# Performance work log

Hardware: AMD Instinct MI355X
Metric: run time of the kernel (lower is better)

Reference implementation:

```python
import jax, jax.numpy as jnp
import numpy as np

B, S, E, H = 4, 2048, 1024, 16
D = E // H


def setup_inputs() -> dict:
    key = jax.random.key(0)
    ks = jax.random.split(key, 8)
    inv = 1.0 / np.sqrt(E)
    return {
        "query": jax.random.normal(ks[0], (B, S, E), dtype=jnp.float32),
        "key": jax.random.normal(ks[1], (B, S, E), dtype=jnp.float32),
        "value": jax.random.normal(ks[2], (B, S, E), dtype=jnp.float32),
        "key_padding_mask": jnp.zeros((B, S), dtype=bool),
        "Wq": jax.random.uniform(ks[3], (E, E), jnp.float32, -inv, inv),
        "Wk": jax.random.uniform(ks[4], (E, E), jnp.float32, -inv, inv),
        "Wv": jax.random.uniform(ks[5], (E, E), jnp.float32, -inv, inv),
        "Wo": jax.random.uniform(ks[6], (E, E), jnp.float32, -inv, inv),
        "gamma": jnp.ones((H,), dtype=jnp.float32),
    }


def reference(query, key, value, key_padding_mask, Wq, Wk, Wv, Wo, gamma):
    b, s, e = query.shape
    h = gamma.shape[0]
    d = e // h
    # torch Linear: x @ W.T ; split into heads -> [b, h, s, d]
    q = (query @ Wq.T).reshape(b, s, h, d).swapaxes(1, 2)
    k = (key @ Wk.T).reshape(b, key.shape[1], h, d).swapaxes(1, 2)
    v = (value @ Wv.T).reshape(b, value.shape[1], h, d).swapaxes(1, 2)
    scores = jnp.einsum("bhqd,bhkd->bhqk", q, k) / jnp.sqrt(jnp.asarray(d, q.dtype))
    scores = jnp.where(key_padding_mask[:, None, None, :], -jnp.inf, scores)
    attn = jax.nn.softmax(scores, axis=-1)  # dropout p=0 in eval-equivalent reference
    out = jnp.einsum("bhqk,bhkd->bhqd", attn, v)
    out = out * gamma[None, :, None, None]  # head-scale
    out = out.swapaxes(1, 2).reshape(b, s, e)
    return out @ Wo.T
```

## Files before the change

### kernel.cpp

```cpp
#include <hip/hip_runtime.h>
#include <hip/hip_bf16.h>
#include <cstdint>

typedef __bf16 bf16;
typedef __bf16 bf16_8 __attribute__((ext_vector_type(8)));
typedef __bf16 bf16_4 __attribute__((ext_vector_type(4)));
typedef float f32_4 __attribute__((ext_vector_type(4)));
typedef short s16x4 __attribute__((ext_vector_type(4)));
typedef short s16x8 __attribute__((ext_vector_type(8)));

#define MFMA_16x16x32(a, b, c) __builtin_amdgcn_mfma_f32_16x16x32_bf16((a), (b), (c), 0, 0, 0)

__device__ __forceinline__ void gll16(const void* g, void* l) {
  __builtin_amdgcn_global_load_lds((const __attribute__((address_space(1))) void*)g,
                                   (__attribute__((address_space(3))) void*)l, 16, 0, 0);
}

__device__ __forceinline__ float exp2fast(float x) {
#if __has_builtin(__builtin_amdgcn_exp2f)
  return __builtin_amdgcn_exp2f(x);
#else
  return __exp2f(x);
#endif
}

__device__ __forceinline__ unsigned bfbits(float x) {
  bf16 b = (bf16)x;
  return (unsigned)__builtin_bit_cast(unsigned short, b);
}

__global__ __launch_bounds__(256) void cvt3(const float* __restrict__ s0,
                                            const float* __restrict__ s1,
                                            const float* __restrict__ s2,
                                            bf16* __restrict__ d0,
                                            bf16* __restrict__ d1,
                                            bf16* __restrict__ d2) {
  const float* srcs[3] = {s0, s1, s2};
  bf16* dsts[3] = {d0, d1, d2};
  const float* src = srcs[blockIdx.y];
  bf16* dst = dsts[blockIdx.y];
  size_t i = ((size_t)blockIdx.x * 256 + threadIdx.x) * 8;
  float4 f0 = *(const float4*)(src + i);
  float4 f1 = *(const float4*)(src + i + 4);
  bf16_8 v;
  v[0] = (bf16)f0.x; v[1] = (bf16)f0.y; v[2] = (bf16)f0.z; v[3] = (bf16)f0.w;
  v[4] = (bf16)f1.x; v[5] = (bf16)f1.y; v[6] = (bf16)f1.z; v[7] = (bf16)f1.w;
  *(bf16_8*)(dst + i) = v;
}

__global__ __launch_bounds__(256) void convert4(const float* __restrict__ w0,
                                                const float* __restrict__ w1,
                                                const float* __restrict__ w2,
                                                const float* __restrict__ w3,
                                                bf16* __restrict__ out, int per) {
  const float* srcs[4] = {w0, w1, w2, w3};
  const float* src = srcs[blockIdx.y];
  bf16* dst = out + (size_t)blockIdx.y * per;
  int i = (blockIdx.x * 256 + threadIdx.x) * 4;
  float4 f = *(const float4*)(src + i);
  bf16_4 v;
  v[0] = (bf16)f.x; v[1] = (bf16)f.y; v[2] = (bf16)f.z; v[3] = (bf16)f.w;
  *(bf16_4*)(dst + i) = v;
}

__global__ __launch_bounds__(256) void gemm_qkv(const bf16* __restrict__ Aq,
                                                const bf16* __restrict__ Ak,
                                                const bf16* __restrict__ Av,
                                                const bf16* __restrict__ W,
                                                bf16* __restrict__ Qp,
                                                bf16* __restrict__ Kp,
                                                bf16* __restrict__ Vt) {
  constexpr int BM = 128, BK = 32, K = 1024, N = 1024, M_S = 2048;
  __shared__ alignas(16) bf16 As[2][BM * BK];
  __shared__ alignas(16) bf16 Bs[2][BM * BK];

  const int tid = threadIdx.x;
  const int wave = tid >> 6, lane = tid & 63;
  const int quad = lane >> 4, l15 = lane & 15;
  const int wm = (wave & 1) * 64, wn = (wave >> 1) * 64;
  const int tensor = blockIdx.y >> 3;
  const int n0 = (blockIdx.y & 7) * 128;
  const size_t m0 = (size_t)blockIdx.x * BM;

  const bf16* A = tensor == 0 ? Aq : (tensor == 1 ? Ak : Av);
  const bf16* Bt = W + ((size_t)tensor << 20);

  f32_4 acc[4][4] = {};

  const size_t g_laneoff = (size_t)(lane >> 2) * K + (lane & 3) * 8;
  const bf16* Ag = A + (m0 + wave * 32) * (size_t)K + g_laneoff;
  const bf16* Bg = Bt + ((size_t)n0 + wave * 32) * (size_t)K + g_laneoff;
  const int l_off = wave * 32 * BK + lane * 8;

  auto stage = [&](int b, int k0) {
    gll16(Ag + k0, &As[b][l_off]);
    gll16(Ag + 16 * (size_t)K + k0, &As[b][l_off + 16 * BK]);
    gll16(Bg + k0, &Bs[b][l_off]);
    gll16(Bg + 16 * (size_t)K + k0, &Bs[b][l_off + 16 * BK]);
  };

  stage(0, 0);
  int buf = 0;
  for (int k0 = 0; k0 < K; k0 += BK, buf ^= 1) {
    __syncthreads();
    if (k0 + BK < K) stage(buf ^ 1, k0 + BK);

    bf16_8 af[4], bfr[4];
#pragma unroll
    for (int mt = 0; mt < 4; ++mt)
      af[mt] = *(const bf16_8*)&As[buf][(wm + mt * 16 + l15) * BK + quad * 8];
#pragma unroll
    for (int nt = 0; nt < 4; ++nt)
      bfr[nt] = *(const bf16_8*)&Bs[buf][(wn + nt * 16 + l15) * BK + quad * 8];
#pragma unroll
    for (int mt = 0; mt < 4; ++mt)
#pragma unroll
      for (int nt = 0; nt < 4; ++nt)
        acc[mt][nt] = MFMA_16x16x32(af[mt], bfr[nt], acc[mt][nt]);
  }

  if (tensor < 2) {
    bf16* C = tensor == 0 ? Qp : Kp;
#pragma unroll
    for (int mt = 0; mt < 4; ++mt)
#pragma unroll
      for (int i = 0; i < 4; ++i) {
        size_t row = m0 + wm + mt * 16 + quad * 4 + i;
        bf16* cr = C + row * N + n0 + wn + l15;
#pragma unroll
        for (int nt = 0; nt < 4; ++nt) cr[nt * 16] = (bf16)acc[mt][nt][i];
      }
  } else {
    const int bb = (int)(m0 >> 11);
    const int sbase = (int)(m0 & 2047) + wm;
#pragma unroll
    for (int mt = 0; mt < 4; ++mt)
#pragma unroll
      for (int nt = 0; nt < 4; ++nt) {
        int col = n0 + wn + nt * 16 + l15;
        bf16_4 pk;
        pk[0] = (bf16)acc[mt][nt][0]; pk[1] = (bf16)acc[mt][nt][1];
        pk[2] = (bf16)acc[mt][nt][2]; pk[3] = (bf16)acc[mt][nt][3];
        bf16* dst = Vt + ((size_t)(bb * 16 + (col >> 6)) * 64 + (col & 63)) * M_S +
                    sbase + (mt >> 1) * 32 + quad * 8 + (mt & 1) * 4;
        *(bf16_4*)dst = pk;
      }
  }
}

__global__ __launch_bounds__(256) void gemm_out(const bf16* __restrict__ A,
                                                const bf16* __restrict__ Bt,
                                                float* __restrict__ C,
                                                int M, int N, int K) {
  constexpr int BM = 128, BN = 128, BK = 32;
  __shared__ alignas(16) bf16 As[2][BM * BK];
  __shared__ alignas(16) bf16 Bs[2][BN * BK];

  const int tid = threadIdx.x;
  const int wave = tid >> 6, lane = tid & 63;
  const int quad = lane >> 4, l15 = lane & 15;
  const int wm = (wave & 1) * 64, wn = (wave >> 1) * 64;
  const size_t m0 = (size_t)blockIdx.x * BM;
  const size_t n0 = (size_t)blockIdx.y * BN;

  f32_4 acc[4][4] = {};

  const size_t g_laneoff = (size_t)(lane >> 2) * K + (lane & 3) * 8;
  const bf16* Ag = A + (m0 + wave * 32) * (size_t)K + g_laneoff;
  const bf16* Bg = Bt + (n0 + wave * 32) * (size_t)K + g_laneoff;
  const int l_off = wave * 32 * BK + lane * 8;

  auto stage = [&](int b, int k0) {
    gll16(Ag + k0, &As[b][l_off]);
    gll16(Ag + 16 * (size_t)K + k0, &As[b][l_off + 16 * BK]);
    gll16(Bg + k0, &Bs[b][l_off]);
    gll16(Bg + 16 * (size_t)K + k0, &Bs[b][l_off + 16 * BK]);
  };

  stage(0, 0);
  int buf = 0;
  for (int k0 = 0; k0 < K; k0 += BK, buf ^= 1) {
    __syncthreads();
    if (k0 + BK < K) stage(buf ^ 1, k0 + BK);

    bf16_8 af[4], bfr[4];
#pragma unroll
    for (int mt = 0; mt < 4; ++mt)
      af[mt] = *(const bf16_8*)&As[buf][(wm + mt * 16 + l15) * BK + quad * 8];
#pragma unroll
    for (int nt = 0; nt < 4; ++nt)
      bfr[nt] = *(const bf16_8*)&Bs[buf][(wn + nt * 16 + l15) * BK + quad * 8];
#pragma unroll
    for (int mt = 0; mt < 4; ++mt)
#pragma unroll
      for (int nt = 0; nt < 4; ++nt)
        acc[mt][nt] = MFMA_16x16x32(af[mt], bfr[nt], acc[mt][nt]);
  }

#pragma unroll
  for (int mt = 0; mt < 4; ++mt)
#pragma unroll
    for (int i = 0; i < 4; ++i) {
      size_t row = m0 + wm + mt * 16 + quad * 4 + i;
      float* cr = C + row * N + n0 + wn + l15;
#pragma unroll
      for (int nt = 0; nt < 4; ++nt) cr[nt * 16] = acc[mt][nt][i];
    }
}

__global__ __launch_bounds__(256, 4) void attn_fused(const bf16* __restrict__ Q,
                                                     const bf16* __restrict__ K,
                                                     const bf16* __restrict__ Vt,
                                                     const unsigned char* __restrict__ mask,
                                                     const float* __restrict__ gamma,
                                                     bf16* __restrict__ Out) {
  constexpr int S = 2048, E = 1024;
  constexpr float scale2 = 0.125f * 1.44269504f;
  constexpr float CB = -10.0f * 1.44269504f;
  constexpr float NEGB = -3.0e38f;
  __shared__ alignas(16) bf16 Ks[2][64 * 64];
  __shared__ alignas(16) bf16 Vs[2][64 * 64];
  __shared__ int s_any;

  const int tid = threadIdx.x;
  const int wave = tid >> 6, lane = tid & 63;
  const int quad = lane >> 4, l15 = lane & 15;
  const int q0 = blockIdx.x * 128;
  const int bh = blockIdx.y;
  const int b = bh >> 4, h = bh & 15;

  const unsigned char* mg = mask + (size_t)b * S;

  if (tid == 0) s_any = 0;
  __syncthreads();
  {
    uint2 mv = ((const uint2*)mg)[tid];
    unsigned long long bal = __ballot((mv.x | mv.y) != 0);
    if (lane == 0 && bal) s_any = 1;
  }
  __syncthreads();
  const bool anym = s_any != 0;

  const int lrow = lane >> 3;
  const int sx = ((lane & 7) ^ lrow) * 8;
  const size_t koff = (size_t)lrow * E + sx;
  const size_t voff = (size_t)lrow * S + sx;

  const bf16* Qg = Q + ((size_t)(b * S + q0)) * E + h * 64;
  const bf16* Kg = K + ((size_t)b * S) * E + h * 64;
  const bf16* Vg = Vt + ((size_t)bh * 64) * S;

  auto stageKV = [&](int bf, int kt) {
#pragma unroll
    for (int p = 0; p < 2; ++p) {
      gll16(Kg + (size_t)(kt + wave * 16 + p * 8) * E + koff,
            &Ks[bf][(wave * 16 + p * 8) * 64 + lane * 8]);
      gll16(Vg + (size_t)(wave * 16 + p * 8) * S + voff + kt,
            &Vs[bf][(wave * 16 + p * 8) * 64 + lane * 8]);
    }
  };

  stageKV(0, 0);

  bf16_8 qf[2][2];
#pragma unroll
  for (int mt = 0; mt < 2; ++mt)
#pragma unroll
    for (int ks = 0; ks < 2; ++ks)
      qf[mt][ks] = *(const bf16_8*)(Qg + (size_t)(wave * 32 + mt * 16 + l15) * E +
                                    ks * 32 + quad * 8);

  s16x8 onesP;
#pragma unroll
  for (int j = 0; j < 8; ++j) onesP[j] = (short)0x3F80;
  const bf16_8 onesA8 = __builtin_bit_cast(bf16_8, onesP);

  f32_4 accO[4][2] = {};
  f32_4 accR[2] = {};

  int buf = 0;
  for (int kt = 0; kt < S; kt += 64, buf ^= 1) {
    __syncthreads();
    if (kt + 64 < S) stageKV(buf ^ 1, kt + 64);

    f32_4 sT[4][2] = {};
#pragma unroll
    for (int ks = 0; ks < 2; ++ks)
#pragma unroll
      for (int t = 0; t < 4; ++t) {
        bf16_8 af = *(const bf16_8*)&Ks[buf][(t * 16 + l15) * 64 +
                                            (((ks * 4 + quad) ^ (l15 & 7)) * 8)];
        sT[t][0] = MFMA_16x16x32(af, qf[0][ks], sT[t][0]);
        sT[t][1] = MFMA_16x16x32(af, qf[1][ks], sT[t][1]);
      }

    s16x4 pk[4][2];
#pragma unroll
    for (int t = 0; t < 4; ++t) {
      float bb0, bb1, bb2, bb3;
      if (anym) {
        const unsigned um = *(const unsigned*)(mg + kt + t * 16 + quad * 4);
        bb0 = (um & 0xffu) ? NEGB : CB;
        bb1 = (um & 0xff00u) ? NEGB : CB;
        bb2 = (um & 0xff0000u) ? NEGB : CB;
        bb3 = (um & 0xff000000u) ? NEGB : CB;
      } else {
        bb0 = bb1 = bb2 = bb3 = CB;
      }
#pragma unroll
      for (int mt = 0; mt < 2; ++mt) {
        float e0 = exp2fast(fmaf(sT[t][mt][0], scale2, bb0));
        float e1 = exp2fast(fmaf(sT[t][mt][1], scale2, bb1));
        float e2 = exp2fast(fmaf(sT[t][mt][2], scale2, bb2));
        float e3 = exp2fast(fmaf(sT[t][mt][3], scale2, bb3));
        uint2 u;
        u.x = bfbits(e0) | (bfbits(e1) << 16);
        u.y = bfbits(e2) | (bfbits(e3) << 16);
        pk[t][mt] = __builtin_bit_cast(s16x4, u);
      }
    }

#pragma unroll
    for (int i2 = 0; i2 < 2; ++i2) {
      const bf16_8 pb0 = __builtin_bit_cast(bf16_8,
          __builtin_shufflevector(pk[2 * i2][0], pk[2 * i2 + 1][0], 0, 1, 2, 3, 4, 5, 6, 7));
      const bf16_8 pb1 = __builtin_bit_cast(bf16_8,
          __builtin_shufflevector(pk[2 * i2][1], pk[2 * i2 + 1][1], 0, 1, 2, 3, 4, 5, 6, 7));
      accR[0] = MFMA_16x16x32(onesA8, pb0, accR[0]);
      accR[1] = MFMA_16x16x32(onesA8, pb1, accR[1]);
      const int c = (i2 * 4 + quad) ^ (l15 & 7);
#pragma unroll
      for (int dt = 0; dt < 4; ++dt) {
        bf16_8 vf = *(const bf16_8*)&Vs[buf][(dt * 16 + l15) * 64 + c * 8];
        accO[dt][0] = MFMA_16x16x32(vf, pb0, accO[dt][0]);
        accO[dt][1] = MFMA_16x16x32(vf, pb1, accO[dt][1]);
      }
    }
  }

  const float g = gamma[h];
  float invv[2];
#pragma unroll
  for (int mt = 0; mt < 2; ++mt) invv[mt] = g / accR[mt][0];

#pragma unroll
  for (int mt = 0; mt < 2; ++mt) {
    size_t token = (size_t)(b * S) + q0 + wave * 32 + mt * 16 + l15;
    bf16* orow = Out + token * E + h * 64;
#pragma unroll
    for (int dt = 0; dt < 4; ++dt) {
      bf16_4 ov;
      ov[0] = (bf16)(accO[dt][mt][0] * invv[mt]);
      ov[1] = (bf16)(accO[dt][mt][1] * invv[mt]);
      ov[2] = (bf16)(accO[dt][mt][2] * invv[mt]);
      ov[3] = (bf16)(accO[dt][mt][3] * invv[mt]);
      *(bf16_4*)(orow + dt * 16 + quad * 4) = ov;
    }
  }
}

extern "C" void kernel_launch(void* const* d_in, const int* in_sizes, int n_in,
                              void* d_out, int out_size, void* d_ws, size_t ws_size,
                              hipStream_t stream) {
  constexpr int Bb = 4, S = 2048, E = 1024;
  constexpr int M = Bb * S;

  const float* q = (const float*)d_in[0];
  const float* k = (const float*)d_in[1];
  const float* v = (const float*)d_in[2];
  const unsigned char* mask = (const unsigned char*)d_in[3];
  const float* Wq = (const float*)d_in[4];
  const float* Wk = (const float*)d_in[5];
  const float* Wv = (const float*)d_in[6];
  const float* Wo = (const float*)d_in[7];
  const float* gamma = (const float*)d_in[8];

  char* ws = (char*)d_ws;
  bf16* Wb = (bf16*)ws;
  bf16* qb = (bf16*)(ws + ((size_t)8 << 20));
  bf16* kb = (bf16*)(ws + ((size_t)24 << 20));
  bf16* vb = (bf16*)(ws + ((size_t)40 << 20));
  bf16* Vt = (bf16*)(ws + ((size_t)56 << 20));
  bf16* Qp = (bf16*)d_out;
  bf16* Kp = (bf16*)d_out + ((size_t)1 << 23);

  convert4<<<dim3(1024, 4), 256, 0, stream>>>(Wq, Wk, Wv, Wo, Wb, 1 << 20);
  cvt3<<<dim3(4096, 3), 256, 0, stream>>>(q, k, v, qb, kb, vb);

  gemm_qkv<<<dim3(M / 128, 24), 256, 0, stream>>>(qb, kb, vb, Wb, Qp, Kp, Vt);

  bf16* At = qb;
  attn_fused<<<dim3(S / 128, Bb * 16), 256, 0, stream>>>(Qp, Kp, Vt, mask, gamma, At);

  gemm_out<<<dim3(M / 128, E / 128), 256, 0, stream>>>(At, Wb + (3 << 20), (float*)d_out, M, E, E);
}
```

Measured before the change: 352.9 us.

## Fuse fp32-to-bf16 activation conversion into QKV GEMM and fold softmax scale into Wq

```diff
diff --git a/kernel.cpp b/kernel.cpp
--- a/kernel.cpp
+++ b/kernel.cpp
@@ -29,23 +29,11 @@
   return (unsigned)__builtin_bit_cast(unsigned short, b);
 }
 
-__global__ __launch_bounds__(256) void cvt3(const float* __restrict__ s0,
-                                            const float* __restrict__ s1,
-                                            const float* __restrict__ s2,
-                                            bf16* __restrict__ d0,
-                                            bf16* __restrict__ d1,
-                                            bf16* __restrict__ d2) {
-  const float* srcs[3] = {s0, s1, s2};
-  bf16* dsts[3] = {d0, d1, d2};
-  const float* src = srcs[blockIdx.y];
-  bf16* dst = dsts[blockIdx.y];
-  size_t i = ((size_t)blockIdx.x * 256 + threadIdx.x) * 8;
-  float4 f0 = *(const float4*)(src + i);
-  float4 f1 = *(const float4*)(src + i + 4);
+__device__ __forceinline__ bf16_8 cvt8(float4 a, float4 b) {
   bf16_8 v;
-  v[0] = (bf16)f0.x; v[1] = (bf16)f0.y; v[2] = (bf16)f0.z; v[3] = (bf16)f0.w;
-  v[4] = (bf16)f1.x; v[5] = (bf16)f1.y; v[6] = (bf16)f1.z; v[7] = (bf16)f1.w;
-  *(bf16_8*)(dst + i) = v;
+  v[0] = (bf16)a.x; v[1] = (bf16)a.y; v[2] = (bf16)a.z; v[3] = (bf16)a.w;
+  v[4] = (bf16)b.x; v[5] = (bf16)b.y; v[6] = (bf16)b.z; v[7] = (bf16)b.w;
+  return v;
 }
 
 __global__ __launch_bounds__(256) void convert4(const float* __restrict__ w0,
@@ -56,16 +44,18 @@
   const float* srcs[4] = {w0, w1, w2, w3};
   const float* src = srcs[blockIdx.y];
   bf16* dst = out + (size_t)blockIdx.y * per;
+  const float sc = (blockIdx.y == 0) ? 0.18033688f : 1.0f;
   int i = (blockIdx.x * 256 + threadIdx.x) * 4;
   float4 f = *(const float4*)(src + i);
   bf16_4 v;
-  v[0] = (bf16)f.x; v[1] = (bf16)f.y; v[2] = (bf16)f.z; v[3] = (bf16)f.w;
+  v[0] = (bf16)(f.x * sc); v[1] = (bf16)(f.y * sc);
+  v[2] = (bf16)(f.z * sc); v[3] = (bf16)(f.w * sc);
   *(bf16_4*)(dst + i) = v;
 }
 
-__global__ __launch_bounds__(256) void gemm_qkv(const bf16* __restrict__ Aq,
-                                                const bf16* __restrict__ Ak,
-                                                const bf16* __restrict__ Av,
+__global__ __launch_bounds__(256) void gemm_qkv(const float* __restrict__ Aq,
+                                                const float* __restrict__ Ak,
+                                                const float* __restrict__ Av,
                                                 const bf16* __restrict__ W,
                                                 bf16* __restrict__ Qp,
                                                 bf16* __restrict__ Kp,
@@ -82,28 +72,46 @@
   const int n0 = (blockIdx.y & 7) * 128;
   const size_t m0 = (size_t)blockIdx.x * BM;
 
-  const bf16* A = tensor == 0 ? Aq : (tensor == 1 ? Ak : Av);
+  const float* A = tensor == 0 ? Aq : (tensor == 1 ? Ak : Av);
   const bf16* Bt = W + ((size_t)tensor << 20);
 
   f32_4 acc[4][4] = {};
 
   const size_t g_laneoff = (size_t)(lane >> 2) * K + (lane & 3) * 8;
-  const bf16* Ag = A + (m0 + wave * 32) * (size_t)K + g_laneoff;
+  const float* Ag = A + (m0 + wave * 32) * (size_t)K + g_laneoff;
   const bf16* Bg = Bt + ((size_t)n0 + wave * 32) * (size_t)K + g_laneoff;
   const int l_off = wave * 32 * BK + lane * 8;
 
-  auto stage = [&](int b, int k0) {
-    gll16(Ag + k0, &As[b][l_off]);
-    gll16(Ag + 16 * (size_t)K + k0, &As[b][l_off + 16 * BK]);
+  auto stageB = [&](int b, int k0) {
     gll16(Bg + k0, &Bs[b][l_off]);
     gll16(Bg + 16 * (size_t)K + k0, &Bs[b][l_off + 16 * BK]);
   };
-
-  stage(0, 0);
+  auto loadA = [&](int k0, float4* r) {
+    r[0] = *(const float4*)(Ag + k0);
+    r[1] = *(const float4*)(Ag + k0 + 4);
+    r[2] = *(const float4*)(Ag + 16 * (size_t)K + k0);
+    r[3] = *(const float4*)(Ag + 16 * (size_t)K + k0 + 4);
+  };
+  auto writeA = [&](int b, const float4* r) {
+    *(bf16_8*)&As[b][l_off] = cvt8(r[0], r[1]);
+    *(bf16_8*)&As[b][l_off + 16 * BK] = cvt8(r[2], r[3]);
+  };
+
+  {
+    float4 a0[4];
+    loadA(0, a0);
+    stageB(0, 0);
+    writeA(0, a0);
+  }
   int buf = 0;
   for (int k0 = 0; k0 < K; k0 += BK, buf ^= 1) {
     __syncthreads();
-    if (k0 + BK < K) stage(buf ^ 1, k0 + BK);
+    const bool more = k0 + BK < K;
+    float4 an[4];
+    if (more) {
+      loadA(k0 + BK, an);
+      stageB(buf ^ 1, k0 + BK);
+    }
 
     bf16_8 af[4], bfr[4];
 #pragma unroll
@@ -117,6 +125,8 @@
 #pragma unroll
       for (int nt = 0; nt < 4; ++nt)
         acc[mt][nt] = MFMA_16x16x32(af[mt], bfr[nt], acc[mt][nt]);
+
+    if (more) writeA(buf ^ 1, an);
   }
 
   if (tensor < 2) {
@@ -215,31 +225,29 @@
                                                      const float* __restrict__ gamma,
                                                      bf16* __restrict__ Out) {
   constexpr int S = 2048, E = 1024;
-  constexpr float scale2 = 0.125f * 1.44269504f;
-  constexpr float CB = -10.0f * 1.44269504f;
   constexpr float NEGB = -3.0e38f;
   __shared__ alignas(16) bf16 Ks[2][64 * 64];
   __shared__ alignas(16) bf16 Vs[2][64 * 64];
-  __shared__ int s_any;
 
   const int tid = threadIdx.x;
   const int wave = tid >> 6, lane = tid & 63;
   const int quad = lane >> 4, l15 = lane & 15;
-  const int q0 = blockIdx.x * 128;
-  const int bh = blockIdx.y;
+
+  const int bx = blockIdx.x, by = blockIdx.y;
+  const int wx = (bx >> 3) | ((by & 7) << 1);
+  const int bh = (bx & 7) | (by & ~7);
+  const int q0 = wx * 128;
   const int b = bh >> 4, h = bh & 15;
 
   const unsigned char* mg = mask + (size_t)b * S;
 
-  if (tid == 0) s_any = 0;
-  __syncthreads();
+  bool anym;
   {
-    uint2 mv = ((const uint2*)mg)[tid];
-    unsigned long long bal = __ballot((mv.x | mv.y) != 0);
-    if (lane == 0 && bal) s_any = 1;
-  }
-  __syncthreads();
-  const bool anym = s_any != 0;
+    const uint4* m4 = (const uint4*)mg;
+    uint4 x = m4[lane * 2], y = m4[lane * 2 + 1];
+    unsigned o = (x.x | x.y | x.z | x.w) | (y.x | y.y | y.z | y.w);
+    anym = __ballot(o != 0) != 0ull;
+  }
 
   const int lrow = lane >> 3;
   const int sx = ((lane & 7) ^ lrow) * 8;
@@ -250,13 +258,13 @@
   const bf16* Kg = K + ((size_t)b * S) * E + h * 64;
   const bf16* Vg = Vt + ((size_t)bh * 64) * S;
 
-  auto stageKV = [&](int bf, int kt) {
+  auto stageKV = [&](int bf_, int kt) {
 #pragma unroll
     for (int p = 0; p < 2; ++p) {
       gll16(Kg + (size_t)(kt + wave * 16 + p * 8) * E + koff,
-            &Ks[bf][(wave * 16 + p * 8) * 64 + lane * 8]);
+            &Ks[bf_][(wave * 16 + p * 8) * 64 + lane * 8]);
       gll16(Vg + (size_t)(wave * 16 + p * 8) * S + voff + kt,
-            &Vs[bf][(wave * 16 + p * 8) * 64 + lane * 8]);
+            &Vs[bf_][(wave * 16 + p * 8) * 64 + lane * 8]);
     }
   };
 
@@ -297,22 +305,20 @@
     s16x4 pk[4][2];
 #pragma unroll
     for (int t = 0; t < 4; ++t) {
-      float bb0, bb1, bb2, bb3;
+      float bb0 = 0.0f, bb1 = 0.0f, bb2 = 0.0f, bb3 = 0.0f;
       if (anym) {
         const unsigned um = *(const unsigned*)(mg + kt + t * 16 + quad * 4);
-        bb0 = (um & 0xffu) ? NEGB : CB;
-        bb1 = (um & 0xff00u) ? NEGB : CB;
-        bb2 = (um & 0xff0000u) ? NEGB : CB;
-        bb3 = (um & 0xff000000u) ? NEGB : CB;
-      } else {
-        bb0 = bb1 = bb2 = bb3 = CB;
+        bb0 = (um & 0xffu) ? NEGB : 0.0f;
+        bb1 = (um & 0xff00u) ? NEGB : 0.0f;
+        bb2 = (um & 0xff0000u) ? NEGB : 0.0f;
+        bb3 = (um & 0xff000000u) ? NEGB : 0.0f;
       }
 #pragma unroll
       for (int mt = 0; mt < 2; ++mt) {
-        float e0 = exp2fast(fmaf(sT[t][mt][0], scale2, bb0));
-        float e1 = exp2fast(fmaf(sT[t][mt][1], scale2, bb1));
-        float e2 = exp2fast(fmaf(sT[t][mt][2], scale2, bb2));
-        float e3 = exp2fast(fmaf(sT[t][mt][3], scale2, bb3));
+        float e0 = exp2fast(sT[t][mt][0] + bb0);
+        float e1 = exp2fast(sT[t][mt][1] + bb1);
+        float e2 = exp2fast(sT[t][mt][2] + bb2);
+        float e3 = exp2fast(sT[t][mt][3] + bb3);
         uint2 u;
         u.x = bfbits(e0) | (bfbits(e1) << 16);
         u.y = bfbits(e2) | (bfbits(e3) << 16);
@@ -328,10 +334,10 @@
           __builtin_shufflevector(pk[2 * i2][1], pk[2 * i2 + 1][1], 0, 1, 2, 3, 4, 5, 6, 7));
       accR[0] = MFMA_16x16x32(onesA8, pb0, accR[0]);
       accR[1] = MFMA_16x16x32(onesA8, pb1, accR[1]);
-      const int c = (i2 * 4 + quad) ^ (l15 & 7);
+      const int xo = ((i2 * 4 + quad) ^ (l15 & 7)) * 8;
 #pragma unroll
       for (int dt = 0; dt < 4; ++dt) {
-        bf16_8 vf = *(const bf16_8*)&Vs[buf][(dt * 16 + l15) * 64 + c * 8];
+        bf16_8 vf = *(const bf16_8*)&Vs[buf][(dt * 16 + l15) * 64 + xo];
         accO[dt][0] = MFMA_16x16x32(vf, pb0, accO[dt][0]);
         accO[dt][1] = MFMA_16x16x32(vf, pb1, accO[dt][1]);
       }
@@ -377,19 +383,15 @@
 
   char* ws = (char*)d_ws;
   bf16* Wb = (bf16*)ws;
-  bf16* qb = (bf16*)(ws + ((size_t)8 << 20));
-  bf16* kb = (bf16*)(ws + ((size_t)24 << 20));
-  bf16* vb = (bf16*)(ws + ((size_t)40 << 20));
+  bf16* At = (bf16*)(ws + ((size_t)8 << 20));
   bf16* Vt = (bf16*)(ws + ((size_t)56 << 20));
   bf16* Qp = (bf16*)d_out;
   bf16* Kp = (bf16*)d_out + ((size_t)1 << 23);
 
   convert4<<<dim3(1024, 4), 256, 0, stream>>>(Wq, Wk, Wv, Wo, Wb, 1 << 20);
-  cvt3<<<dim3(4096, 3), 256, 0, stream>>>(q, k, v, qb, kb, vb);
-
-  gemm_qkv<<<dim3(M / 128, 24), 256, 0, stream>>>(qb, kb, vb, Wb, Qp, Kp, Vt);
-
-  bf16* At = qb;
+
+  gemm_qkv<<<dim3(M / 128, 24), 256, 0, stream>>>(q, k, v, Wb, Qp, Kp, Vt);
+
   attn_fused<<<dim3(S / 128, Bb * 16), 256, 0, stream>>>(Qp, Kp, Vt, mask, gamma, At);
 
   gemm_out<<<dim3(M / 128, E / 128), 256, 0, stream>>>(At, Wb + (3 << 20), (float*)d_out, M, E, E);
```

Measured after the change: 396.0 us. 12.2% more time.
